# Optimization experiments

Hardware: AMD Instinct MI355X
Metric: run time of the kernel (lower is better)

Reference implementation:

```python
import jax, jax.numpy as jnp
import numpy as np

RNN = 64      # rnn_hidden_dim
HID = 64      # hidden_dim
ENC = 3       # encoder_dim
NAG = 8       # n_agents
NACT = 14     # n_actions
CLIP = 0.2    # args.exp_clip (variance floor)
BN_EPS = 1e-5


def _bn(x, g, b):
    # BatchNorm1d in training mode: batch stats, biased variance
    m = x.mean(0)
    v = jnp.mean((x - m) ** 2, 0)
    return g * (x - m) * jax.lax.rsqrt(v + BN_EPS) + b


def setup_inputs() -> dict:
    key = jax.random.key(0)
    ks = jax.random.split(key, 16)
    B, INP = 8192, 96

    def w(k, shape, fan):
        return (jax.random.normal(k, shape, jnp.float32) / np.float32(np.sqrt(fan)))

    d = {}
    d["inputs"] = jax.random.normal(ks[0], (B * NAG, INP), jnp.float32)
    d["hidden_state"] = jax.random.normal(ks[1], (B * NAG, RNN), jnp.float32)
    d["noise"] = jax.random.normal(ks[2], (B, NAG, NAG * ENC), jnp.float32)
    d["fc1_w"] = w(ks[3], (INP, RNN), INP); d["fc1_b"] = jnp.zeros((RNN,), jnp.float32)
    d["w_ih"] = w(ks[4], (RNN, 3 * RNN), RNN); d["w_hh"] = w(ks[5], (RNN, 3 * RNN), RNN)
    d["b_ih"] = jnp.zeros((3 * RNN,), jnp.float32); d["b_hh"] = jnp.zeros((3 * RNN,), jnp.float32)
    d["aw1_w"] = w(ks[6], (RNN, HID), RNN); d["aw1_b"] = jnp.zeros((HID,), jnp.float32)
    d["aw_g"] = jnp.ones((HID,), jnp.float32); d["aw_be"] = jnp.zeros((HID,), jnp.float32)
    d["aw2_w"] = w(ks[7], (HID, 2 * NAG * ENC), HID); d["aw2_b"] = jnp.zeros((2 * NAG * ENC,), jnp.float32)
    d["po1_w"] = w(ks[8], (2 * RNN, HID), 2 * RNN); d["po1_b"] = jnp.zeros((HID,), jnp.float32)
    d["po_g"] = jnp.ones((HID,), jnp.float32); d["po_be"] = jnp.zeros((HID,), jnp.float32)
    d["po2_w"] = w(ks[9], (HID, 2 * ENC), HID); d["po2_b"] = jnp.zeros((2 * ENC,), jnp.float32)
    d["fc2_w"] = w(ks[10], (RNN + ENC * NAG, NACT), RNN + ENC * NAG); d["fc2_b"] = jnp.zeros((NACT,), jnp.float32)
    return d


def reference(inputs, hidden_state, noise,
              fc1_w, fc1_b, w_ih, w_hh, b_ih, b_hh,
              aw1_w, aw1_b, aw_g, aw_be, aw2_w, aw2_b,
              po1_w, po1_b, po_g, po_be, po2_w, po2_b,
              fc2_w, fc2_b):
    B, n, enc = noise.shape[0], NAG, ENC

    x = jax.nn.relu(inputs @ fc1_w + fc1_b)                      # [B*n, RNN]
    h_in = hidden_state.reshape(-1, RNN)

    # torch GRUCell
    gi = x @ w_ih + b_ih
    gh = h_in @ w_hh + b_hh
    ir, iz, i_n = jnp.split(gi, 3, axis=-1)
    hr, hz, h_n = jnp.split(gh, 3, axis=-1)
    r = jax.nn.sigmoid(ir + hr)
    z = jax.nn.sigmoid(iz + hz)
    nt = jnp.tanh(i_n + r * h_n)
    h = (1.0 - z) * nt + z * h_in                                # [B*n, RNN]

    # awareness encoder
    a = jax.nn.relu(_bn(h @ aw1_w + aw1_b, aw_g, aw_be))
    aw = (a @ aw2_w + aw2_b).reshape(B, n, 2 * n * enc)
    mu = aw[:, :, : n * enc]
    sigma = jnp.maximum(jnp.exp(aw[:, :, n * enc:]), CLIP)       # variance
    c = (mu + jnp.sqrt(sigma) * noise).reshape(-1, n * enc)      # rsample

    x_out = jnp.concatenate([h, c], axis=-1) @ fc2_w + fc2_b     # [B*n, NACT]

    # poster branch (training mode): all-pairs concat H[b, j, id] = [h[b,id], h[b,j]]
    hd = jax.lax.stop_gradient(h).reshape(B, n, RNN)
    Hi = jnp.broadcast_to(hd[:, None, :, :], (B, n, n, RNN))     # axis2 = id
    Hj = jnp.broadcast_to(hd[:, :, None, :], (B, n, n, RNN))     # axis1 = j
    H = jnp.concatenate([Hi, Hj], axis=-1).reshape(-1, 2 * RNN)  # [B*n*n, 2*RNN]

    p = jax.nn.relu(_bn(H @ po1_w + po1_b, po_g, po_be))
    out = (p @ po2_w + po2_b).reshape(B, n, 2 * n * enc)
    mu1 = out[:, :, : n * enc]
    sigma1 = jnp.maximum(jnp.exp(out[:, :, n * enc:]), CLIP)

    # KL between diagonal Gaussians (sigma, sigma1 are variances)
    kl = 0.5 * (jnp.log(sigma1 / sigma) + (sigma + (mu - mu1) ** 2) / sigma1 - 1.0)
    KL = kl.mean(axis=-1).mean(axis=-1, keepdims=True)           # [B, 1]
    return (x_out, h, KL)
```

## Files before the change

### kernel.cpp

```cpp
#include <hip/hip_runtime.h>
#include <math.h>

#define NROWS 65536
#define NB    8192
#define STAT_OFF  0
#define WPACK_OFF 3584
#define OUT_XOUT 0
#define OUT_H    917504
#define OUT_KL   5111808

typedef __attribute__((ext_vector_type(8))) short bhalf8;
typedef __attribute__((ext_vector_type(4))) float floatx4;
typedef __attribute__((ext_vector_type(4))) unsigned short u16x4;

__device__ __forceinline__ float sigmf(float x) { return 1.0f / (1.0f + __expf(-x)); }
__device__ __forceinline__ float tanhfast(float x) {
    x = fminf(fmaxf(x, -15.f), 15.f);
    float e = __expf(-2.f * x);
    return (1.f - e) / (1.f + e);
}
__device__ __forceinline__ unsigned short f2bf(float f) {
    unsigned int u = __float_as_uint(f);
    u += 0x7FFFu + ((u >> 16) & 1u);
    return (unsigned short)(u >> 16);
}
__device__ __forceinline__ float bf2f(unsigned short s) {
    return __uint_as_float(((unsigned int)s) << 16);
}
__device__ __forceinline__ bhalf8 pack8(float4 a, float4 b) {
    bhalf8 r;
    r[0] = (short)f2bf(a.x); r[1] = (short)f2bf(a.y);
    r[2] = (short)f2bf(a.z); r[3] = (short)f2bf(a.w);
    r[4] = (short)f2bf(b.x); r[5] = (short)f2bf(b.y);
    r[6] = (short)f2bf(b.z); r[7] = (short)f2bf(b.w);
    return r;
}

__device__ __forceinline__ int p2idx(int g, int i) {
    switch (i) {
        case 0:  return (0 + g) * 2 + 0;   case 1:  return (0 + g) * 2 + 1;
        case 2:  return (12 + g) * 2 + 0;  case 3:  return (12 + g) * 2 + 1;
        case 4:  return (4 + g) * 2 + 0;   case 5:  return (4 + g) * 2 + 1;
        case 6:  return (16 + g) * 2 + 0;  case 7:  return (16 + g) * 2 + 1;
        case 8:  return (8 + g) * 2 + 0;   case 9:  return (8 + g) * 2 + 1;
        case 10: return (20 + g) * 2 + 0;  default: return (20 + g) * 2 + 1;
    }
}
__device__ __forceinline__ int p3idx(int g, int i) {
    switch (i) {
        case 0: return g * 2 + 0;        case 1: return g * 2 + 1;
        case 2: return (4 + g) * 2 + 0;  case 3: return (4 + g) * 2 + 1;
        case 4: return (8 + g) * 2 + 0;  default: return (8 + g) * 2 + 1;
    }
}

__global__ void k_prep(const float* __restrict__ fc1_w,
                       const float* __restrict__ w_ih, const float* __restrict__ w_hh,
                       const float* __restrict__ aw1_w, const float* __restrict__ po1_w,
                       const float* __restrict__ aw2_w, const float* __restrict__ fc2_w,
                       float* __restrict__ ws)
{
    const int t = threadIdx.x;
    if (blockIdx.x == 0)
        for (int i = t; i < 3584; i += 64) ws[STAT_OFF + i] = 0.f;

    unsigned short* wpk = (unsigned short*)(ws + WPACK_OFF);
    int f = blockIdx.x * 64 + t;
    if (f < 5952) {
        int lane, c, tile;
        const float* src;
        int colbase, krowstride, kofs = 0, kmax = 1 << 30, colmax = 16;
        if (f < 768) {
            tile = f / 192; c = (f % 192) / 64; lane = f % 64;
            src = fc1_w; krowstride = 64; colbase = tile * 16;
        } else if (f < 3840) {
            int f2 = f - 768;
            tile = f2 / 128; c = (f2 % 128) / 64; lane = f2 % 64;
            if (tile < 12) { src = w_ih; colbase = tile * 16; }
            else           { src = w_hh; colbase = (tile - 12) * 16; }
            krowstride = 192;
        } else if (f < 5376) {
            int f3 = f - 3840;
            tile = f3 / 128; c = (f3 % 128) / 64; lane = f3 % 64;
            if (tile < 4)       { src = aw1_w; colbase = tile * 16; }
            else if (tile < 8)  { src = po1_w; colbase = (tile - 4) * 16; }
            else                { src = po1_w; colbase = (tile - 8) * 16; kofs = 64; }
            krowstride = 64;
        } else if (f < 5760) {
            int f4 = f - 5376;
            tile = f4 / 128; c = (f4 % 128) / 64; lane = f4 % 64;
            src = aw2_w; krowstride = 48; colbase = tile * 16;
        } else {
            int f5 = f - 5760;
            c = f5 / 64; lane = f5 % 64;
            src = fc2_w; krowstride = 14; colbase = 0;
            kmax = 88; colmax = 14;
        }
        int n = lane & 15, quad = lane >> 4;
        int col = colbase + n;
        unsigned short o[8];
        #pragma unroll
        for (int j = 0; j < 8; j++) {
            int k = c * 32 + quad * 8 + j + kofs;
            float v = (k < kmax && n < colmax) ? src[(size_t)k * krowstride + col] : 0.f;
            o[j] = f2bf(v);
        }
        u16x4 lo, hi;
        lo.x = o[0]; lo.y = o[1]; lo.z = o[2]; lo.w = o[3];
        hi.x = o[4]; hi.y = o[5]; hi.z = o[6]; hi.w = o[7];
        *(u16x4*)&wpk[f * 8]     = lo;
        *(u16x4*)&wpk[f * 8 + 4] = hi;
    }
}

__global__ __launch_bounds__(256, 2) void k_front(
    const float* __restrict__ inp, const float* __restrict__ hin,
    const float* __restrict__ fc1_b,
    const float* __restrict__ b_ih, const float* __restrict__ b_hh,
    const float* __restrict__ aw1_b,
    float* __restrict__ h_out, float* __restrict__ ws)
{
    __shared__ __align__(16) unsigned short s_xb[128 * 80];
    __shared__ float s_stat[448];

    const int t = threadIdx.x;
    const int row0 = blockIdx.x * 128;
    const int lane = t & 63;
    const int w = t >> 6;
    const int n16 = lane & 15;
    const int quad = lane >> 4;

    for (int i = t; i < 448; i += 256) s_stat[i] = 0.f;
    __syncthreads();

    const bhalf8* wp1 = (const bhalf8*)((const unsigned short*)(ws + WPACK_OFF));
    const bhalf8* wp2 = wp1 + 768;
    const bhalf8* wp3 = wp1 + 3840;

    bhalf8 ai[2][3], ahf[2][2];
    #pragma unroll
    for (int u = 0; u < 2; u++) {
        const float* gi = inp + (size_t)(row0 + w * 32 + u * 16 + n16) * 96 + quad * 8;
        #pragma unroll
        for (int kc = 0; kc < 3; kc++)
            ai[u][kc] = pack8(*(const float4*)&gi[kc * 32], *(const float4*)&gi[kc * 32 + 4]);
        const float* gh = hin + (size_t)(row0 + w * 32 + u * 16 + n16) * 64 + quad * 8;
        #pragma unroll
        for (int kc = 0; kc < 2; kc++)
            ahf[u][kc] = pack8(*(const float4*)&gh[kc * 32], *(const float4*)&gh[kc * 32 + 4]);
    }

    float b1v[4], brv[4], bzv[4], binv[4], bhnv[4], abv[4];
    #pragma unroll
    for (int g = 0; g < 4; g++) {
        int col = g * 16 + n16;
        b1v[g]  = fc1_b[col];
        brv[g]  = b_ih[col] + b_hh[col];
        bzv[g]  = b_ih[64 + col] + b_hh[64 + col];
        binv[g] = b_ih[128 + col];
        bhnv[g] = b_hh[128 + col];
        abv[g]  = aw1_b[col];
    }

    bhalf8 f1a[2][3];
    #pragma unroll
    for (int i = 0; i < 3; i++) f1a[0][i] = wp1[i * 64 + lane];
    #pragma unroll
    for (int g = 0; g < 4; g++) {
        const int cur = g & 1, nxt = cur ^ 1;
        if (g < 3) {
            #pragma unroll
            for (int i = 0; i < 3; i++) f1a[nxt][i] = wp1[((g + 1) * 3 + i) * 64 + lane];
        }
        int col = g * 16 + n16;
        #pragma unroll
        for (int u = 0; u < 2; u++) {
            floatx4 d = {0.f, 0.f, 0.f, 0.f};
            d = __builtin_amdgcn_mfma_f32_16x16x32_bf16(ai[u][0], f1a[cur][0], d, 0, 0, 0);
            d = __builtin_amdgcn_mfma_f32_16x16x32_bf16(ai[u][1], f1a[cur][1], d, 0, 0, 0);
            d = __builtin_amdgcn_mfma_f32_16x16x32_bf16(ai[u][2], f1a[cur][2], d, 0, 0, 0);
            #pragma unroll
            for (int q = 0; q < 4; q++)
                s_xb[(w * 32 + u * 16 + quad * 4 + q) * 80 + col] = f2bf(fmaxf(d[q] + b1v[g], 0.f));
        }
    }

    bhalf8 f2a[2][12];
    float hpv[2][8];
    #pragma unroll
    for (int i = 0; i < 12; i++) f2a[0][i] = wp2[p2idx(0, i) * 64 + lane];
    #pragma unroll
    for (int u = 0; u < 2; u++)
        #pragma unroll
        for (int q = 0; q < 4; q++)
            hpv[0][u * 4 + q] = hin[(size_t)(row0 + w * 32 + u * 16 + quad * 4 + q) * 64 + n16];

    bhalf8 ax[2][2];
    #pragma unroll
    for (int u = 0; u < 2; u++) {
        int mr = w * 32 + u * 16 + n16;
        ax[u][0] = *(const bhalf8*)&s_xb[mr * 80 + 0  + quad * 8];
        ax[u][1] = *(const bhalf8*)&s_xb[mr * 80 + 32 + quad * 8];
    }

    #pragma unroll
    for (int g = 0; g < 4; g++) {
        const int cur = g & 1, nxt = cur ^ 1;
        if (g < 3) {
            #pragma unroll
            for (int i = 0; i < 12; i++) f2a[nxt][i] = wp2[p2idx(g + 1, i) * 64 + lane];
            #pragma unroll
            for (int u = 0; u < 2; u++)
                #pragma unroll
                for (int q = 0; q < 4; q++)
                    hpv[nxt][u * 4 + q] = hin[(size_t)(row0 + w * 32 + u * 16 + quad * 4 + q) * 64 + (g + 1) * 16 + n16];
        }
        int col = g * 16 + n16;
        floatx4 dr[2], dz[2], dn[2], dh[2];
        #pragma unroll
        for (int u = 0; u < 2; u++) {
            floatx4 d = {0.f, 0.f, 0.f, 0.f};
            d = __builtin_amdgcn_mfma_f32_16x16x32_bf16(ax[u][0], f2a[cur][0], d, 0, 0, 0);
            d = __builtin_amdgcn_mfma_f32_16x16x32_bf16(ax[u][1], f2a[cur][1], d, 0, 0, 0);
            d = __builtin_amdgcn_mfma_f32_16x16x32_bf16(ahf[u][0], f2a[cur][2], d, 0, 0, 0);
            d = __builtin_amdgcn_mfma_f32_16x16x32_bf16(ahf[u][1], f2a[cur][3], d, 0, 0, 0);
            dr[u] = d;
            floatx4 e = {0.f, 0.f, 0.f, 0.f};
            e = __builtin_amdgcn_mfma_f32_16x16x32_bf16(ax[u][0], f2a[cur][4], e, 0, 0, 0);
            e = __builtin_amdgcn_mfma_f32_16x16x32_bf16(ax[u][1], f2a[cur][5], e, 0, 0, 0);
            e = __builtin_amdgcn_mfma_f32_16x16x32_bf16(ahf[u][0], f2a[cur][6], e, 0, 0, 0);
            e = __builtin_amdgcn_mfma_f32_16x16x32_bf16(ahf[u][1], f2a[cur][7], e, 0, 0, 0);
            dz[u] = e;
            floatx4 f = {0.f, 0.f, 0.f, 0.f};
            f = __builtin_amdgcn_mfma_f32_16x16x32_bf16(ax[u][0], f2a[cur][8], f, 0, 0, 0);
            f = __builtin_amdgcn_mfma_f32_16x16x32_bf16(ax[u][1], f2a[cur][9], f, 0, 0, 0);
            dn[u] = f;
            floatx4 h4 = {0.f, 0.f, 0.f, 0.f};
            h4 = __builtin_amdgcn_mfma_f32_16x16x32_bf16(ahf[u][0], f2a[cur][10], h4, 0, 0, 0);
            h4 = __builtin_amdgcn_mfma_f32_16x16x32_bf16(ahf[u][1], f2a[cur][11], h4, 0, 0, 0);
            dh[u] = h4;
        }
        #pragma unroll
        for (int u = 0; u < 2; u++) {
            #pragma unroll
            for (int q = 0; q < 4; q++) {
                int lrow = w * 32 + u * 16 + quad * 4 + q;
                size_t grow = (size_t)(row0 + lrow);
                float r  = sigmf(dr[u][q] + brv[g]);
                float z  = sigmf(dz[u][q] + bzv[g]);
                float nt = tanhfast(dn[u][q] + binv[g] + r * (dh[u][q] + bhnv[g]));
                float hp = hpv[cur][u * 4 + q];
                float h  = (1.f - z) * nt + z * hp;
                h_out[grow * 64 + col] = h;
                s_xb[lrow * 80 + col] = f2bf(h);
            }
        }
    }

    bhalf8 f3a[2][6];
    #pragma unroll
    for (int i = 0; i < 6; i++) f3a[0][i] = wp3[p3idx(0, i) * 64 + lane];

    bhalf8 hh[2][2];
    #pragma unroll
    for (int u = 0; u < 2; u++) {
        int mr = w * 32 + u * 16 + n16;
        hh[u][0] = *(const bhalf8*)&s_xb[mr * 80 + 0  + quad * 8];
        hh[u][1] = *(const bhalf8*)&s_xb[mr * 80 + 32 + quad * 8];
    }

    #pragma unroll
    for (int g = 0; g < 4; g++) {
        const int cur = g & 1, nxt = cur ^ 1;
        if (g < 3) {
            #pragma unroll
            for (int i = 0; i < 6; i++) f3a[nxt][i] = wp3[p3idx(g + 1, i) * 64 + lane];
        }
        int col = g * 16 + n16;
        floatx4 da[2], du[2], dvv[2];
        #pragma unroll
        for (int u = 0; u < 2; u++) {
            floatx4 d = {0.f, 0.f, 0.f, 0.f};
            d = __builtin_amdgcn_mfma_f32_16x16x32_bf16(hh[u][0], f3a[cur][0], d, 0, 0, 0);
            d = __builtin_amdgcn_mfma_f32_16x16x32_bf16(hh[u][1], f3a[cur][1], d, 0, 0, 0);
            da[u] = d;
            floatx4 e = {0.f, 0.f, 0.f, 0.f};
            e = __builtin_amdgcn_mfma_f32_16x16x32_bf16(hh[u][0], f3a[cur][2], e, 0, 0, 0);
            e = __builtin_amdgcn_mfma_f32_16x16x32_bf16(hh[u][1], f3a[cur][3], e, 0, 0, 0);
            du[u] = e;
            floatx4 f = {0.f, 0.f, 0.f, 0.f};
            f = __builtin_amdgcn_mfma_f32_16x16x32_bf16(hh[u][0], f3a[cur][4], f, 0, 0, 0);
            f = __builtin_amdgcn_mfma_f32_16x16x32_bf16(hh[u][1], f3a[cur][5], f, 0, 0, 0);
            dvv[u] = f;
        }
        float ab = abv[g];
        float s1 = 0.f, s2 = 0.f, suq = 0.f, svq = 0.f;
        float su[2] = {0.f, 0.f}, sv[2] = {0.f, 0.f};
        #pragma unroll
        for (int u = 0; u < 2; u++) {
            #pragma unroll
            for (int q = 0; q < 4; q++) {
                float a = da[u][q] + ab; s1 += a; s2 += a * a;
                float uv = du[u][q]; su[u] += uv; suq += uv * uv;
                float vv = dvv[u][q]; sv[u] += vv; svq += vv * vv;
            }
        }
        #pragma unroll
        for (int u = 0; u < 2; u++) {
            float u8 = su[u] + __shfl_xor(su[u], 16, 64);
            float v8 = sv[u] + __shfl_xor(sv[u], 16, 64);
            if ((quad & 1) == 0)
                atomicAdd(&s_stat[384 + col], u8 * v8 * (1.f / 64.f));
        }
        float sut = su[0] + su[1];
        float svt = sv[0] + sv[1];
        float t1 = s1 + __shfl_xor(s1, 16, 64);   t1 += __shfl_xor(t1, 32, 64);
        float t2 = s2 + __shfl_xor(s2, 16, 64);   t2 += __shfl_xor(t2, 32, 64);
        float t3 = sut + __shfl_xor(sut, 16, 64); t3 += __shfl_xor(t3, 32, 64);
        float t4 = suq + __shfl_xor(suq, 16, 64); t4 += __shfl_xor(t4, 32, 64);
        float t5 = svt + __shfl_xor(svt, 16, 64); t5 += __shfl_xor(t5, 32, 64);
        float t6 = svq + __shfl_xor(svq, 16, 64); t6 += __shfl_xor(t6, 32, 64);
        if (quad == 0) {
            atomicAdd(&s_stat[col], t1);
            atomicAdd(&s_stat[64 + col], t2);
            atomicAdd(&s_stat[128 + col], t3);
            atomicAdd(&s_stat[192 + col], t4);
            atomicAdd(&s_stat[256 + col], t5);
            atomicAdd(&s_stat[320 + col], t6);
        }
    }
    __syncthreads();
    if (t < 64) {
        float* gs = ws + STAT_OFF + (blockIdx.x & 7) * 448;
        #pragma unroll
        for (int q = 0; q < 7; q++)
            atomicAdd(&gs[q * 64 + t], s_stat[q * 64 + t]);
    }
}

__global__ __launch_bounds__(128) void k_heads(
    const float* __restrict__ h_glob, const float* __restrict__ noise,
    const float* __restrict__ aw1_b, const float* __restrict__ aw2_b,
    const float* __restrict__ fc2_b, const float* __restrict__ po2_b,
    const float* __restrict__ aw_g, const float* __restrict__ aw_be,
    const float* __restrict__ po_g, const float* __restrict__ po_be,
    const float* __restrict__ po1_b, const float* __restrict__ po2_w,
    const float* __restrict__ ws, float* __restrict__ out)
{
    __shared__ __align__(16) unsigned short s_hb[32 * 104];
    __shared__ __align__(16) unsigned short s_Ub[32 * 80];
    __shared__ __align__(16) unsigned short s_Vb[32 * 80];
    __shared__ float s_ms[32 * 48];
    __shared__ __align__(16) float s_out[32 * 48];
    __shared__ __align__(16) float s_dv[640];
    __shared__ float s_kl[32];

    const int t = threadIdx.x;
    const int row0 = blockIdx.x * 32;
    const int b0 = blockIdx.x * 4;
    const int lane = t & 63;
    const int w = t >> 6;
    const int n16 = lane & 15;
    const int quad = lane >> 4;
    const int mrow = w * 16 + n16;

    if (t < 64) {
        const float* st = ws + STAT_OFF;
        float sa = 0.f, sb = 0.f, sc = 0.f, sd = 0.f, se = 0.f, sf = 0.f, sg = 0.f;
        #pragma unroll
        for (int r = 0; r < 8; r++) {
            const float* sr = st + r * 448;
            sa += sr[t];       sb += sr[64 + t];  sc += sr[128 + t];
            sd += sr[192 + t]; se += sr[256 + t]; sf += sr[320 + t];
            sg += sr[384 + t];
        }
        const float invN = 1.f / 65536.f;
        float am = sa * invN;
        float av = sb * invN - am * am;
        float asc = aw_g[t] * rsqrtf(av + 1e-5f);
        s_dv[t] = asc;
        s_dv[64 + t] = aw_be[t] - asc * am;
        float Eu = sc * invN;
        float vu = sd * invN - Eu * Eu;
        float Ev = se * invN;
        float vv = sf * invN - Ev * Ev;
        float cov = sg * (1.f / 8192.f) - Eu * Ev;
        float my = Eu + Ev + po1_b[t];
        float vy = vu + vv + 2.f * cov;
        float psc = po_g[t] * rsqrtf(vy + 1e-5f);
        s_dv[128 + t] = psc;
        s_dv[192 + t] = po_be[t] + psc * (po1_b[t] - my);
    }
    for (int i = t; i < 384; i += 128) {
        int d = i >> 6, c = i & 63;
        s_dv[256 + i] = po2_w[c * 6 + d];
    }

    const bhalf8* wp3  = ((const bhalf8*)((const unsigned short*)(ws + WPACK_OFF))) + 3840;
    const bhalf8* wpa2 = wp3 + 1536;
    const bhalf8* wpf2 = wpa2 + 384;

    float abv[4];
    #pragma unroll
    for (int g = 0; g < 4; g++) abv[g] = aw1_b[g * 16 + n16];

    {
        const float* gh = h_glob + (size_t)row0 * 64;
        for (int i = t; i < 512; i += 128) {
            int r = i >> 4, c4 = (i & 15) * 4;
            float4 v = *(const float4*)&gh[r * 64 + c4];
            u16x4 p; p.x = f2bf(v.x); p.y = f2bf(v.y); p.z = f2bf(v.z); p.w = f2bf(v.w);
            *(u16x4*)&s_hb[r * 104 + c4] = p;
        }
        for (int i = t; i < 64; i += 128) {
            int r = i >> 1, c4 = 88 + (i & 1) * 4;
            u16x4 z; z.x = 0; z.y = 0; z.z = 0; z.w = 0;
            *(u16x4*)&s_hb[r * 104 + c4] = z;
        }
    }

    bhalf8 fA[2][6];
    #pragma unroll
    for (int i = 0; i < 6; i++) fA[0][i] = wp3[p3idx(0, i) * 64 + lane];

    __syncthreads();

    unsigned short* s_ab = (unsigned short*)s_out;

    float ascv[4], ashv[4], pscv[4], pshv[4];
    #pragma unroll
    for (int g = 0; g < 4; g++) {
        int col = g * 16 + n16;
        ascv[g] = s_dv[col];       ashv[g] = s_dv[64 + col];
        pscv[g] = s_dv[128 + col]; pshv[g] = s_dv[192 + col];
    }

    {
        bhalf8 ah0 = *(const bhalf8*)&s_hb[mrow * 104 + 0  + quad * 8];
        bhalf8 ah1 = *(const bhalf8*)&s_hb[mrow * 104 + 32 + quad * 8];
        #pragma unroll
        for (int g = 0; g < 4; g++) {
            const int cur = g & 1, nxt = cur ^ 1;
            if (g < 3) {
                #pragma unroll
                for (int i = 0; i < 6; i++) fA[nxt][i] = wp3[p3idx(g + 1, i) * 64 + lane];
            }
            int col = g * 16 + n16;
            floatx4 da = {0.f, 0.f, 0.f, 0.f}, duu = {0.f, 0.f, 0.f, 0.f}, dvv = {0.f, 0.f, 0.f, 0.f};
            da  = __builtin_amdgcn_mfma_f32_16x16x32_bf16(ah0, fA[cur][0], da, 0, 0, 0);
            da  = __builtin_amdgcn_mfma_f32_16x16x32_bf16(ah1, fA[cur][1], da, 0, 0, 0);
            duu = __builtin_amdgcn_mfma_f32_16x16x32_bf16(ah0, fA[cur][2], duu, 0, 0, 0);
            duu = __builtin_amdgcn_mfma_f32_16x16x32_bf16(ah1, fA[cur][3], duu, 0, 0, 0);
            dvv = __builtin_amdgcn_mfma_f32_16x16x32_bf16(ah0, fA[cur][4], dvv, 0, 0, 0);
            dvv = __builtin_amdgcn_mfma_f32_16x16x32_bf16(ah1, fA[cur][5], dvv, 0, 0, 0);
            #pragma unroll
            for (int q = 0; q < 4; q++) {
                int lrow = w * 16 + quad * 4 + q;
                s_ab[lrow * 80 + col] = f2bf(fmaxf(ascv[g] * (da[q] + abv[g]) + ashv[g], 0.f));
                s_Ub[lrow * 80 + col] = f2bf(pscv[g] * duu[q]);
                s_Vb[lrow * 80 + col] = f2bf(pscv[g] * dvv[q] + pshv[g]);
            }
        }
    }

    {
        bhalf8 fB[2][2];
        fB[0][0] = wpa2[0 * 64 + lane];
        fB[0][1] = wpa2[1 * 64 + lane];
        float bbv[3];
        #pragma unroll
        for (int g = 0; g < 3; g++) bbv[g] = aw2_b[g * 16 + n16];

        bhalf8 aa0 = *(const bhalf8*)&s_ab[mrow * 80 + 0  + quad * 8];
        bhalf8 aa1 = *(const bhalf8*)&s_ab[mrow * 80 + 32 + quad * 8];
        #pragma unroll
        for (int g = 0; g < 3; g++) {
            const int cur = g & 1, nxt = cur ^ 1;
            if (g < 2) {
                fB[nxt][0] = wpa2[((g + 1) * 2 + 0) * 64 + lane];
                fB[nxt][1] = wpa2[((g + 1) * 2 + 1) * 64 + lane];
            }
            floatx4 d = {0.f, 0.f, 0.f, 0.f};
            d = __builtin_amdgcn_mfma_f32_16x16x32_bf16(aa0, fB[cur][0], d, 0, 0, 0);
            d = __builtin_amdgcn_mfma_f32_16x16x32_bf16(aa1, fB[cur][1], d, 0, 0, 0);
            int col = g * 16 + n16;
            #pragma unroll
            for (int q = 0; q < 4; q++) {
                int lrow = w * 16 + quad * 4 + q;
                float v = d[q] + bbv[g];
                s_ms[lrow * 48 + col] = (col < 24) ? v : fmaxf(__expf(v), 0.2f);
            }
        }
    }

    bhalf8 ff[3];
    ff[0] = wpf2[0 * 64 + lane];
    ff[1] = wpf2[1 * 64 + lane];
    ff[2] = wpf2[2 * 64 + lane];

    __syncthreads();

    for (int i = t; i < 768; i += 128) {
        int r = i / 24, m = i - r * 24;
        float c = s_ms[r * 48 + m] + sqrtf(s_ms[r * 48 + 24 + m]) * noise[(size_t)(row0 + r) * 24 + m];
        s_hb[r * 104 + 64 + m] = f2bf(c);
    }
    __syncthreads();

    {
        bhalf8 hc0 = *(const bhalf8*)&s_hb[mrow * 104 + 0  + quad * 8];
        bhalf8 hc1 = *(const bhalf8*)&s_hb[mrow * 104 + 32 + quad * 8];
        bhalf8 hc2 = *(const bhalf8*)&s_hb[mrow * 104 + 64 + quad * 8];
        floatx4 d = {0.f, 0.f, 0.f, 0.f};
        d = __builtin_amdgcn_mfma_f32_16x16x32_bf16(hc0, ff[0], d, 0, 0, 0);
        d = __builtin_amdgcn_mfma_f32_16x16x32_bf16(hc1, ff[1], d, 0, 0, 0);
        d = __builtin_amdgcn_mfma_f32_16x16x32_bf16(hc2, ff[2], d, 0, 0, 0);
        if (n16 < 14) {
            float bb = fc2_b[n16];
            float* xout = out + OUT_XOUT;
            #pragma unroll
            for (int q = 0; q < 4; q++) {
                size_t grow = (size_t)(row0 + w * 16 + quad * 4 + q);
                xout[grow * 14 + n16] = d[q] + bb;
            }
        }
    }
    __syncthreads();

    {
        const float* p2t = s_dv + 256;
        const int bl = t >> 5;
        const int rem = t & 31;
        const int i_ = rem >> 2;
        const int j0 = (rem & 3) * 2;
        float acc[2][6];
        #pragma unroll
        for (int jj = 0; jj < 2; jj++)
            #pragma unroll
            for (int d = 0; d < 6; d++) acc[jj][d] = 0.f;

        for (int c = 0; c < 64; c += 4) {
            u16x4 vb4 = *(const u16x4*)&s_Vb[(bl * 8 + i_) * 80 + c];
            float vv[4] = {bf2f(vb4.x), bf2f(vb4.y), bf2f(vb4.z), bf2f(vb4.w)};
            float wv[6][4];
            #pragma unroll
            for (int d = 0; d < 6; d++) *(float4*)wv[d] = *(const float4*)&p2t[d * 64 + c];
            #pragma unroll
            for (int jj = 0; jj < 2; jj++) {
                u16x4 ub4 = *(const u16x4*)&s_Ub[(bl * 8 + j0 + jj) * 80 + c];
                float p[4];
                p[0] = fmaxf(bf2f(ub4.x) + vv[0], 0.f);
                p[1] = fmaxf(bf2f(ub4.y) + vv[1], 0.f);
                p[2] = fmaxf(bf2f(ub4.z) + vv[2], 0.f);
                p[3] = fmaxf(bf2f(ub4.w) + vv[3], 0.f);
                #pragma unroll
                for (int d = 0; d < 6; d++)
                    acc[jj][d] += p[0] * wv[d][0] + p[1] * wv[d][1] + p[2] * wv[d][2] + p[3] * wv[d][3];
            }
        }
        #pragma unroll
        for (int jj = 0; jj < 2; jj++)
            #pragma unroll
            for (int d = 0; d < 6; d++)
                s_out[(bl * 8 + i_) * 48 + (j0 + jj) * 6 + d] = acc[jj][d] + po2_b[d];
    }
    __syncthreads();

    if (t < 32) {
        float s = 0.f;
        #pragma unroll 4
        for (int m = 0; m < 24; m++) {
            float mu0 = s_ms[t * 48 + m];
            float sg0 = s_ms[t * 48 + 24 + m];
            float mu1 = s_out[t * 48 + m];
            float sg1 = fmaxf(__expf(s_out[t * 48 + 24 + m]), 0.2f);
            float d0 = mu0 - mu1;
            s += __logf(sg1 / sg0) + (sg0 + d0 * d0) / sg1 - 1.f;
        }
        s_kl[t] = s;
    }
    __syncthreads();
    if (t < 4) {
        float s = 0.f;
        #pragma unroll
        for (int i = 0; i < 8; i++) s += s_kl[t * 8 + i];
        out[OUT_KL + b0 + t] = s * (0.5f / 192.f);
    }
}

extern "C" void kernel_launch(void* const* d_in, const int* in_sizes, int n_in,
                              void* d_out, int out_size, void* d_ws, size_t ws_size,
                              hipStream_t stream)
{
    (void)in_sizes; (void)n_in; (void)out_size; (void)ws_size;
    const float* inp   = (const float*)d_in[0];
    const float* hin   = (const float*)d_in[1];
    const float* noise = (const float*)d_in[2];
    const float* fc1_w = (const float*)d_in[3];
    const float* fc1_b = (const float*)d_in[4];
    const float* w_ih  = (const float*)d_in[5];
    const float* w_hh  = (const float*)d_in[6];
    const float* b_ih  = (const float*)d_in[7];
    const float* b_hh  = (const float*)d_in[8];
    const float* aw1_w = (const float*)d_in[9];
    const float* aw1_b = (const float*)d_in[10];
    const float* aw_g  = (const float*)d_in[11];
    const float* aw_be = (const float*)d_in[12];
    const float* aw2_w = (const float*)d_in[13];
    const float* aw2_b = (const float*)d_in[14];
    const float* po1_w = (const float*)d_in[15];
    const float* po1_b = (const float*)d_in[16];
    const float* po_g  = (const float*)d_in[17];
    const float* po_be = (const float*)d_in[18];
    const float* po2_w = (const float*)d_in[19];
    const float* po2_b = (const float*)d_in[20];
    const float* fc2_w = (const float*)d_in[21];
    const float* fc2_b = (const float*)d_in[22];
    float* out = (float*)d_out;
    float* ws  = (float*)d_ws;

    hipLaunchKernelGGL(k_prep,  dim3(93),   dim3(64), 0, stream,
                       fc1_w, w_ih, w_hh, aw1_w, po1_w, aw2_w, fc2_w, ws);
    hipLaunchKernelGGL(k_front, dim3(512),  dim3(256), 0, stream,
                       inp, hin, fc1_b, b_ih, b_hh, aw1_b, out + OUT_H, ws);
    hipLaunchKernelGGL(k_heads, dim3(2048), dim3(128), 0, stream,
                       out + OUT_H, noise, aw1_b, aw2_b, fc2_b, po2_b,
                       aw_g, aw_be, po_g, po_be, po1_b, po2_w, ws, out);
}
```

Before: 181.8 us.

## Run poster pairwise po2 projection on bf16 MFMA with swizzled LDS layout

Replaces the scalar FP32 all-pairs relu(U+V)·po2_w loop in k_heads with bf16 16x16x32 MFMA tiles. The relu(U_j+V_i) operand is built in registers and packed to bf16, and po2_w is pre-packed into the workspace by k_prep. U/V/ab tiles in LDS get an XOR column swizzle, and s_ms is padded, both to cut bank conflicts. This removes a large share of the VALU FMA work per block, at the cost of bf16 rounding on the pairwise activations and the output-layer weights.

```diff
diff --git a/kernel.cpp b/kernel.cpp
--- a/kernel.cpp
+++ b/kernel.cpp
@@ -12,6 +12,7 @@
 typedef __attribute__((ext_vector_type(8))) short bhalf8;
 typedef __attribute__((ext_vector_type(4))) float floatx4;
 typedef __attribute__((ext_vector_type(4))) unsigned short u16x4;
+typedef __attribute__((ext_vector_type(4))) unsigned int u32x4;
 
 __device__ __forceinline__ float sigmf(float x) { return 1.0f / (1.0f + __expf(-x)); }
 __device__ __forceinline__ float tanhfast(float x) {
@@ -34,6 +35,9 @@
     r[4] = (short)f2bf(b.x); r[5] = (short)f2bf(b.y);
     r[6] = (short)f2bf(b.z); r[7] = (short)f2bf(b.w);
     return r;
+}
+__device__ __forceinline__ int swzc(int row, int col) {
+    return col ^ (((row >> 2) & 3) << 4);
 }
 
 __device__ __forceinline__ int p2idx(int g, int i) {
@@ -58,6 +62,7 @@
                        const float* __restrict__ w_ih, const float* __restrict__ w_hh,
                        const float* __restrict__ aw1_w, const float* __restrict__ po1_w,
                        const float* __restrict__ aw2_w, const float* __restrict__ fc2_w,
+                       const float* __restrict__ po2_w,
                        float* __restrict__ ws)
 {
     const int t = threadIdx.x;
@@ -66,7 +71,7 @@
 
     unsigned short* wpk = (unsigned short*)(ws + WPACK_OFF);
     int f = blockIdx.x * 64 + t;
-    if (f < 5952) {
+    if (f < 6080) {
         int lane, c, tile;
         const float* src;
         int colbase, krowstride, kofs = 0, kmax = 1 << 30, colmax = 16;
@@ -90,11 +95,16 @@
             int f4 = f - 5376;
             tile = f4 / 128; c = (f4 % 128) / 64; lane = f4 % 64;
             src = aw2_w; krowstride = 48; colbase = tile * 16;
-        } else {
+        } else if (f < 5952) {
             int f5 = f - 5760;
             c = f5 / 64; lane = f5 % 64;
             src = fc2_w; krowstride = 14; colbase = 0;
             kmax = 88; colmax = 14;
+        } else {
+            int f6 = f - 5952;
+            c = f6 / 64; lane = f6 % 64;
+            src = po2_w; krowstride = 6; colbase = 0;
+            kmax = 64; colmax = 6;
         }
         int n = lane & 15, quad = lane >> 4;
         int col = colbase + n;
@@ -344,15 +354,15 @@
     const float* __restrict__ fc2_b, const float* __restrict__ po2_b,
     const float* __restrict__ aw_g, const float* __restrict__ aw_be,
     const float* __restrict__ po_g, const float* __restrict__ po_be,
-    const float* __restrict__ po1_b, const float* __restrict__ po2_w,
+    const float* __restrict__ po1_b,
     const float* __restrict__ ws, float* __restrict__ out)
 {
     __shared__ __align__(16) unsigned short s_hb[32 * 104];
     __shared__ __align__(16) unsigned short s_Ub[32 * 80];
     __shared__ __align__(16) unsigned short s_Vb[32 * 80];
-    __shared__ float s_ms[32 * 48];
+    __shared__ float s_ms[32 * 52];
     __shared__ __align__(16) float s_out[32 * 48];
-    __shared__ __align__(16) float s_dv[640];
+    __shared__ __align__(16) float s_dv[256];
     __shared__ float s_kl[32];
 
     const int t = threadIdx.x;
@@ -391,18 +401,16 @@
         s_dv[128 + t] = psc;
         s_dv[192 + t] = po_be[t] + psc * (po1_b[t] - my);
     }
-    for (int i = t; i < 384; i += 128) {
-        int d = i >> 6, c = i & 63;
-        s_dv[256 + i] = po2_w[c * 6 + d];
-    }
 
     const bhalf8* wp3  = ((const bhalf8*)((const unsigned short*)(ws + WPACK_OFF))) + 3840;
     const bhalf8* wpa2 = wp3 + 1536;
     const bhalf8* wpf2 = wpa2 + 384;
+    const bhalf8* wpp2 = wpf2 + 192;
 
     float abv[4];
     #pragma unroll
     for (int g = 0; g < 4; g++) abv[g] = aw1_b[g * 16 + n16];
+    float p2bv = (n16 < 6) ? po2_b[n16] : 0.f;
 
     {
         const float* gh = h_glob + (size_t)row0 * 64;
@@ -453,12 +461,13 @@
             duu = __builtin_amdgcn_mfma_f32_16x16x32_bf16(ah1, fA[cur][3], duu, 0, 0, 0);
             dvv = __builtin_amdgcn_mfma_f32_16x16x32_bf16(ah0, fA[cur][4], dvv, 0, 0, 0);
             dvv = __builtin_amdgcn_mfma_f32_16x16x32_bf16(ah1, fA[cur][5], dvv, 0, 0, 0);
+            int scol = col ^ (quad << 4);
             #pragma unroll
             for (int q = 0; q < 4; q++) {
                 int lrow = w * 16 + quad * 4 + q;
-                s_ab[lrow * 80 + col] = f2bf(fmaxf(ascv[g] * (da[q] + abv[g]) + ashv[g], 0.f));
-                s_Ub[lrow * 80 + col] = f2bf(pscv[g] * duu[q]);
-                s_Vb[lrow * 80 + col] = f2bf(pscv[g] * dvv[q] + pshv[g]);
+                s_ab[lrow * 80 + scol] = f2bf(fmaxf(ascv[g] * (da[q] + abv[g]) + ashv[g], 0.f));
+                s_Ub[lrow * 80 + scol] = f2bf(pscv[g] * duu[q]);
+                s_Vb[lrow * 80 + scol] = f2bf(pscv[g] * dvv[q] + pshv[g]);
             }
         }
     }
@@ -471,8 +480,9 @@
         #pragma unroll
         for (int g = 0; g < 3; g++) bbv[g] = aw2_b[g * 16 + n16];
 
-        bhalf8 aa0 = *(const bhalf8*)&s_ab[mrow * 80 + 0  + quad * 8];
-        bhalf8 aa1 = *(const bhalf8*)&s_ab[mrow * 80 + 32 + quad * 8];
+        int anib = ((n16 >> 2) & 3) << 4;
+        bhalf8 aa0 = *(const bhalf8*)&s_ab[mrow * 80 + ((0  + quad * 8) ^ anib)];
+        bhalf8 aa1 = *(const bhalf8*)&s_ab[mrow * 80 + ((32 + quad * 8) ^ anib)];
         #pragma unroll
         for (int g = 0; g < 3; g++) {
             const int cur = g & 1, nxt = cur ^ 1;
@@ -488,7 +498,7 @@
             for (int q = 0; q < 4; q++) {
                 int lrow = w * 16 + quad * 4 + q;
                 float v = d[q] + bbv[g];
-                s_ms[lrow * 48 + col] = (col < 24) ? v : fmaxf(__expf(v), 0.2f);
+                s_ms[lrow * 52 + col] = (col < 24) ? v : fmaxf(__expf(v), 0.2f);
             }
         }
     }
@@ -497,12 +507,14 @@
     ff[0] = wpf2[0 * 64 + lane];
     ff[1] = wpf2[1 * 64 + lane];
     ff[2] = wpf2[2 * 64 + lane];
+    bhalf8 w0 = wpp2[0 * 64 + lane];
+    bhalf8 w1 = wpp2[1 * 64 + lane];
 
     __syncthreads();
 
     for (int i = t; i < 768; i += 128) {
         int r = i / 24, m = i - r * 24;
-        float c = s_ms[r * 48 + m] + sqrtf(s_ms[r * 48 + 24 + m]) * noise[(size_t)(row0 + r) * 24 + m];
+        float c = s_ms[r * 52 + m] + sqrtf(s_ms[r * 52 + 24 + m]) * noise[(size_t)(row0 + r) * 24 + m];
         s_hb[r * 104 + 64 + m] = f2bf(c);
     }
     __syncthreads();
@@ -528,41 +540,39 @@
     __syncthreads();
 
     {
-        const float* p2t = s_dv + 256;
-        const int bl = t >> 5;
-        const int rem = t & 31;
-        const int i_ = rem >> 2;
-        const int j0 = (rem & 3) * 2;
-        float acc[2][6];
-        #pragma unroll
-        for (int jj = 0; jj < 2; jj++)
-            #pragma unroll
-            for (int d = 0; d < 6; d++) acc[jj][d] = 0.f;
-
-        for (int c = 0; c < 64; c += 4) {
-            u16x4 vb4 = *(const u16x4*)&s_Vb[(bl * 8 + i_) * 80 + c];
-            float vv[4] = {bf2f(vb4.x), bf2f(vb4.y), bf2f(vb4.z), bf2f(vb4.w)};
-            float wv[6][4];
-            #pragma unroll
-            for (int d = 0; d < 6; d++) *(float4*)wv[d] = *(const float4*)&p2t[d * 64 + c];
-            #pragma unroll
-            for (int jj = 0; jj < 2; jj++) {
-                u16x4 ub4 = *(const u16x4*)&s_Ub[(bl * 8 + j0 + jj) * 80 + c];
-                float p[4];
-                p[0] = fmaxf(bf2f(ub4.x) + vv[0], 0.f);
-                p[1] = fmaxf(bf2f(ub4.y) + vv[1], 0.f);
-                p[2] = fmaxf(bf2f(ub4.z) + vv[2], 0.f);
-                p[3] = fmaxf(bf2f(ub4.w) + vv[3], 0.f);
+        #pragma unroll
+        for (int tt = 0; tt < 8; tt++) {
+            int tile = w * 8 + tt;
+            int p = tile * 16 + n16;
+            int bl = p >> 6, ii = (p >> 3) & 7, jj = p & 7;
+            int ru = bl * 8 + jj, rv = bl * 8 + ii;
+            int nu = ((ru >> 2) & 3) << 4, nv = ((rv >> 2) & 3) << 4;
+            floatx4 d = {0.f, 0.f, 0.f, 0.f};
+            #pragma unroll
+            for (int kc = 0; kc < 2; kc++) {
+                bhalf8 u8 = *(const bhalf8*)&s_Ub[ru * 80 + ((kc * 32 + quad * 8) ^ nu)];
+                bhalf8 v8 = *(const bhalf8*)&s_Vb[rv * 80 + ((kc * 32 + quad * 8) ^ nv)];
+                u32x4 pw;
                 #pragma unroll
-                for (int d = 0; d < 6; d++)
-                    acc[jj][d] += p[0] * wv[d][0] + p[1] * wv[d][1] + p[2] * wv[d][2] + p[3] * wv[d][3];
-            }
-        }
-        #pragma unroll
-        for (int jj = 0; jj < 2; jj++)
-            #pragma unroll
-            for (int d = 0; d < 6; d++)
-                s_out[(bl * 8 + i_) * 48 + (j0 + jj) * 6 + d] = acc[jj][d] + po2_b[d];
+                for (int m = 0; m < 8; m += 2) {
+                    float lo = fmaxf(bf2f((unsigned short)u8[m])     + bf2f((unsigned short)v8[m]),     0.f);
+                    float hi = fmaxf(bf2f((unsigned short)u8[m + 1]) + bf2f((unsigned short)v8[m + 1]), 0.f);
+                    unsigned int pk;
+                    asm("v_cvt_pk_bf16_f32 %0, %1, %2" : "=v"(pk) : "v"(lo), "v"(hi));
+                    pw[m >> 1] = pk;
+                }
+                bhalf8 pa = __builtin_bit_cast(bhalf8, pw);
+                d = __builtin_amdgcn_mfma_f32_16x16x32_bf16(pa, kc == 0 ? w0 : w1, d, 0, 0, 0);
+            }
+            if (n16 < 6) {
+                #pragma unroll
+                for (int q = 0; q < 4; q++) {
+                    int pr = tile * 16 + quad * 4 + q;
+                    int obl = pr >> 6, oi = (pr >> 3) & 7, oj = pr & 7;
+                    s_out[(obl * 8 + oi) * 48 + oj * 6 + n16] = d[q] + p2bv;
+                }
+            }
+        }
     }
     __syncthreads();
 
@@ -570,8 +580,8 @@
         float s = 0.f;
         #pragma unroll 4
         for (int m = 0; m < 24; m++) {
-            float mu0 = s_ms[t * 48 + m];
-            float sg0 = s_ms[t * 48 + 24 + m];
+            float mu0 = s_ms[t * 52 + m];
+            float sg0 = s_ms[t * 52 + 24 + m];
             float mu1 = s_out[t * 48 + m];
             float sg1 = fmaxf(__expf(s_out[t * 48 + 24 + m]), 0.2f);
             float d0 = mu0 - mu1;
@@ -619,11 +629,11 @@
     float* out = (float*)d_out;
     float* ws  = (float*)d_ws;
 
-    hipLaunchKernelGGL(k_prep,  dim3(93),   dim3(64), 0, stream,
-                       fc1_w, w_ih, w_hh, aw1_w, po1_w, aw2_w, fc2_w, ws);
+    hipLaunchKernelGGL(k_prep,  dim3(95),   dim3(64), 0, stream,
+                       fc1_w, w_ih, w_hh, aw1_w, po1_w, aw2_w, fc2_w, po2_w, ws);
     hipLaunchKernelGGL(k_front, dim3(512),  dim3(256), 0, stream,
                        inp, hin, fc1_b, b_ih, b_hh, aw1_b, out + OUT_H, ws);
     hipLaunchKernelGGL(k_heads, dim3(2048), dim3(128), 0, stream,
                        out + OUT_H, noise, aw1_b, aw2_b, fc2_b, po2_b,
-                       aw_g, aw_be, po_g, po_be, po1_b, po2_w, ws, out);
-}
+                       aw_g, aw_be, po_g, po_be, po1_b, ws, out);
+}
```

Result: faster. 176.0 us (-3.2%).
